# Kernel tuning notes

Hardware: AMD Instinct MI355X
Metric: run time of the kernel (lower is better)

Reference implementation:

```python
import jax, jax.numpy as jnp
import numpy as np

EMB = 1024; H = 8; HD = EMB // H // 2  # head_dim = 64, q/k use 2*H heads of HD; v uses H heads of 2*HD
FF = 4096; DEPTH = 1
LAM_INIT = float(0.8 - 0.6 * np.exp(-0.3 * DEPTH))

def setup_inputs() -> dict:
    key = jax.random.key(0)
    ks = jax.random.split(key, 12)
    s = lambda k, sh, sc: jax.random.normal(k, sh, jnp.float32) * sc
    return {
        'x': s(ks[0], (2, 2048, EMB), 1.0),
        'ln1_w': jnp.ones((EMB,), jnp.float32), 'ln1_b': jnp.zeros((EMB,), jnp.float32),
        'Wq': s(ks[1], (EMB, EMB), 0.02), 'Wk': s(ks[2], (EMB, EMB), 0.02),
        'Wv': s(ks[3], (EMB, EMB), 0.02), 'Wo': s(ks[4], (EMB, EMB), 0.02),
        'lq1': s(ks[5], (HD,), 0.1), 'lk1': s(ks[6], (HD,), 0.1),
        'lq2': s(ks[7], (HD,), 0.1), 'lk2': s(ks[8], (HD,), 0.1),
        'subln_w': jnp.ones((2 * HD,), jnp.float32),
        'ln2_w': jnp.ones((EMB,), jnp.float32), 'ln2_b': jnp.zeros((EMB,), jnp.float32),
        'W1': s(ks[9], (EMB, FF), 0.02), 'b1': jnp.zeros((FF,), jnp.float32),
        'W2': s(ks[10], (FF, EMB), 0.02), 'b2': jnp.zeros((EMB,), jnp.float32),
    }

def _ln(x, w, b):
    m = jnp.mean(x, -1, keepdims=True)
    v = jnp.var(x, -1, keepdims=True)
    return (x - m) * jax.lax.rsqrt(v + 1e-5) * w + b

def _rms(x, w):
    return x * jax.lax.rsqrt(jnp.mean(x * x, -1, keepdims=True) + 1e-5) * w

def reference(x, ln1_w, ln1_b, Wq, Wk, Wv, Wo, lq1, lk1, lq2, lk2, subln_w, ln2_w, ln2_b, W1, b1, W2, b2):
    B, N, _ = x.shape
    h = _ln(x, ln1_w, ln1_b)
    q = (h @ Wq).reshape(B, N, 2 * H, HD) * (HD ** -0.5)
    k = (h @ Wk).reshape(B, N, 2 * H, HD)
    v = (h @ Wv).reshape(B, N, H, 2 * HD)
    # dual softmax attention maps: [B, 2H, N, N]
    attn = jax.nn.softmax(jnp.einsum('bihd,bjhd->bhij', q, k), axis=-1)
    attn = attn.reshape(B, H, 2, N, N)
    lam = jnp.exp(jnp.sum(lq1 * lk1)) - jnp.exp(jnp.sum(lq2 * lk2)) + LAM_INIT
    a = attn[:, :, 0] - lam * attn[:, :, 1]  # differential attention [B,H,N,N]
    o = jnp.einsum('bhij,bjhd->bihd', a, v)  # [B,N,H,2*HD]
    o = _rms(o, subln_w) * (1.0 - LAM_INIT)
    x = x + o.reshape(B, N, EMB) @ Wo
    h = _ln(x, ln2_w, ln2_b)
    return x + (jax.nn.gelu(h @ W1 + b1, approximate=False) @ W2 + b2)
```

## Files before the change

### kernel.cpp

```cpp
#include <hip/hip_runtime.h>


typedef unsigned short u16;
typedef unsigned int u32;
typedef __attribute__((ext_vector_type(8))) __bf16 bf16x8;
typedef __attribute__((ext_vector_type(4))) float f32x4;
typedef __attribute__((ext_vector_type(4))) u32 u32x4;
typedef __attribute__((ext_vector_type(2))) u32 u32x2;

#define LOG2E 1.4426950408889634f
#define LAM_INIT 0.355509068f
#define ONE_MINUS_LAM_INIT 0.644490932f

__device__ __forceinline__ float bf2f(u16 x) {
  u32 u = ((u32)x) << 16;
  return __builtin_bit_cast(float, u);
}
__device__ __forceinline__ u16 f2bf(float f) {
  u32 u = __builtin_bit_cast(u32, f);
  u32 r = (u + 0x7FFFu + ((u >> 16) & 1u)) >> 16;
  return (u16)r;
}
__device__ __forceinline__ u32 cvtpk(float lo, float hi) {
  u32 r;
  asm("v_cvt_pk_bf16_f32 %0, %1, %2" : "=v"(r) : "v"(lo), "v"(hi));
  return r;
}
__device__ __forceinline__ float ldf(const void* p, size_t i, bool f32) {
  return f32 ? ((const float*)p)[i] : bf2f(((const u16*)p)[i]);
}
__device__ __forceinline__ void async16(const u16* g, u16* l) {
  __builtin_amdgcn_global_load_lds((const __attribute__((address_space(1))) u32*)g,
                                   (__attribute__((address_space(3))) u32*)l, 16, 0, 0);
}
__device__ __forceinline__ bf16x8 ld8(const u16* p) { return *(const bf16x8*)p; }

__global__ void detect_kernel(const u32* x, int* flag) {
  int e = (x[threadIdx.x] >> 7) & 0xFF;
  unsigned long long m = __ballot(e >= 90 && e <= 150);
  if (threadIdx.x == 0) flag[0] = (__popcll(m) >= 40) ? 1 : 0;
}

__global__ void lam_kernel(const void* lq1, const void* lk1, const void* lq2,
                           const void* lk2, const int* flag, float* out) {
  const bool f32 = flag[0] == 0;
  int L = threadIdx.x;
  float a = ldf(lq1, L, f32) * ldf(lk1, L, f32);
  float c = ldf(lq2, L, f32) * ldf(lk2, L, f32);
#pragma unroll
  for (int m = 1; m < 64; m <<= 1) { a += __shfl_xor(a, m); c += __shfl_xor(c, m); }
  if (L == 0) out[0] = __expf(a) - __expf(c) + LAM_INIT;
}

__device__ __forceinline__ void unpack8(u32x4 u, float* f) {
#pragma unroll
  for (int i = 0; i < 4; ++i) {
    f[2 * i] = bf2f((u16)(u[i] & 0xffffu));
    f[2 * i + 1] = bf2f((u16)(u[i] >> 16));
  }
}

template <bool XRAW>
__global__ __launch_bounds__(256) void ln_kernel(const void* __restrict__ x,
                                                 const void* __restrict__ w,
                                                 const void* __restrict__ b,
                                                 const int* __restrict__ flag,
                                                 u16* __restrict__ out) {
  const bool f32 = flag[0] == 0;
  const int row = blockIdx.x * 4 + (threadIdx.x >> 6);
  const int L = threadIdx.x & 63;
  float xv[16];
  if (XRAW && f32) {
    const f32x4* xr = (const f32x4*)((const float*)x + (size_t)row * 1024 + L * 16);
#pragma unroll
    for (int i = 0; i < 4; ++i) {
      f32x4 vv = xr[i];
#pragma unroll
      for (int j = 0; j < 4; ++j) xv[i * 4 + j] = vv[j];
    }
  } else {
    const u16* xr = (const u16*)x + (size_t)row * 1024 + L * 16;
    unpack8(*(const u32x4*)xr, xv);
    unpack8(*(const u32x4*)(xr + 8), xv + 8);
  }
  float s = 0.f, sq = 0.f;
#pragma unroll
  for (int i = 0; i < 16; ++i) { s += xv[i]; sq += xv[i] * xv[i]; }
#pragma unroll
  for (int m = 1; m < 64; m <<= 1) { s += __shfl_xor(s, m); sq += __shfl_xor(sq, m); }
  float mean = s * (1.0f / 1024.0f);
  float var = sq * (1.0f / 1024.0f) - mean * mean;
  float rstd = rsqrtf(var + 1e-5f);
  u32 pk[8];
#pragma unroll
  for (int i = 0; i < 8; ++i) {
    float w0 = ldf(w, L * 16 + 2 * i, f32), w1 = ldf(w, L * 16 + 2 * i + 1, f32);
    float b0 = ldf(b, L * 16 + 2 * i, f32), b1v = ldf(b, L * 16 + 2 * i + 1, f32);
    float v0 = (xv[2 * i] - mean) * rstd * w0 + b0;
    float v1 = (xv[2 * i + 1] - mean) * rstd * w1 + b1v;
    pk[i] = (u32)f2bf(v0) | ((u32)f2bf(v1) << 16);
  }
  u32x4 o0 = {pk[0], pk[1], pk[2], pk[3]};
  u32x4 o1 = {pk[4], pk[5], pk[6], pk[7]};
  *(u32x4*)(out + (size_t)row * 1024 + L * 16) = o0;
  *(u32x4*)(out + (size_t)row * 1024 + L * 16 + 8) = o1;
}

__global__ __launch_bounds__(256) void twc_kernel(const void* __restrict__ s0,
                                                  const void* __restrict__ s1,
                                                  const void* __restrict__ s2,
                                                  u16* __restrict__ dst, int sstride,
                                                  int dstride, size_t soff, size_t dzoff,
                                                  const int* __restrict__ flag) {
  __shared__ __align__(16) u16 tile[64][72];
  const bool f32 = flag[0] == 0;
  const void* src = blockIdx.z == 0 ? s0 : (blockIdx.z == 1 ? s1 : s2);
  u16* dz = dst + (size_t)blockIdx.z * dzoff;
  const int r0 = blockIdx.y * 64, c0 = blockIdx.x * 64;
  const int t = threadIdx.x;
  const int rr = t >> 3, cc = t & 7;
#pragma unroll
  for (int i = 0; i < 2; ++i) {
    int row = rr + i * 32;
    size_t idx = (size_t)(r0 + row) * sstride + c0 + cc * 8 + soff;
    if (f32) {
      const f32x4* s = (const f32x4*)((const float*)src + idx);
      f32x4 a = s[0], b = s[1];
      union { u16 t16[8]; u32x4 v; } u_;
#pragma unroll
      for (int j = 0; j < 4; ++j) { u_.t16[j] = f2bf(a[j]); u_.t16[4 + j] = f2bf(b[j]); }
      *(u32x4*)(&tile[row][cc * 8]) = u_.v;
    } else {
      *(u32x4*)(&tile[row][cc * 8]) = *(const u32x4*)((const u16*)src + idx);
    }
  }
  __syncthreads();
  u16* d = dz + (size_t)c0 * dstride + r0;
#pragma unroll
  for (int i = 0; i < 2; ++i) {
    int n = rr + i * 32;
    union { u16 t16[8]; u32x4 v; } u_;
#pragma unroll
    for (int j = 0; j < 8; ++j) u_.t16[j] = tile[cc * 8 + j][n];
    *(u32x4*)(d + (size_t)n * dstride + cc * 8) = u_.v;
  }
}

enum { EP_NONE = 0, EP_RES = 2, EP_GELU = 3, EP_BIASRES = 4, EP_QKV = 5 };

template <int TM, int EPI, bool RESRAW, bool OUTFLEX, bool DB>
__global__ __launch_bounds__(256, 2) void gemm_bt(
    const u16* __restrict__ A, const u16* __restrict__ Bt, void* __restrict__ Cv,
    int M, int N, int K, const void* __restrict__ bias, int boff,
    const void* __restrict__ res, const int* __restrict__ flag,
    u16* __restrict__ kout, u16* __restrict__ vtout) {
  constexpr int MT = TM / 32;
  constexpr int HALF = TM * 64 + 128 * 64;
  extern __shared__ __align__(16) u16 lds[];
  const int t = threadIdx.x;
  const int w = t >> 6, L = t & 63;
  const int quad = L >> 4, l16 = L & 15;
  const int m0 = blockIdx.y * TM, n0 = blockIdx.x * 128;
  const int wm = (TM == 128) ? (w >> 1) * 64 : (w & 1) * 32;
  const int wn = (TM == 128) ? (w & 1) * 64 : (w >> 1) * 64;
  const int srow = L >> 3, spc = L & 7;
  const int sc = spc ^ srow;

  f32x4 acc[MT][4] = {};
  const u16* Ab = A + (size_t)m0 * K;
  const u16* Bb = Bt + (size_t)n0 * K;

  auto stage = [&](int kt, int bsel) {
    u16* base = lds + bsel * HALF;
#pragma unroll
    for (int r = 0; r < TM / 32; ++r) {
      int row = r * 32 + w * 8 + srow;
      async16(Ab + (size_t)row * K + kt + sc * 8, &base[row * 64 + spc * 8]);
    }
#pragma unroll
    for (int r = 0; r < 4; ++r) {
      int row = r * 32 + w * 8 + srow;
      async16(Bb + (size_t)row * K + kt + sc * 8, &base[TM * 64 + row * 64 + spc * 8]);
    }
  };
  auto ktile = [&](const u16* base) {
#pragma unroll
    for (int ks = 0; ks < 2; ++ks) {
      bf16x8 af[MT], bfr[4];
#pragma unroll
      for (int mt = 0; mt < MT; ++mt) {
        int row = wm + mt * 16 + l16;
        af[mt] = ld8(&base[row * 64 + (((ks * 4 + quad) ^ (l16 & 7)) * 8)]);
      }
#pragma unroll
      for (int nt = 0; nt < 4; ++nt) {
        int row = wn + nt * 16 + l16;
        bfr[nt] = ld8(&base[TM * 64 + row * 64 + (((ks * 4 + quad) ^ (l16 & 7)) * 8)]);
      }
#pragma unroll
      for (int mt = 0; mt < MT; ++mt)
#pragma unroll
        for (int nt = 0; nt < 4; ++nt)
          acc[mt][nt] =
              __builtin_amdgcn_mfma_f32_16x16x32_bf16(af[mt], bfr[nt], acc[mt][nt], 0, 0, 0);
    }
  };

  if (DB) {
    const int nst = K >> 6;
    stage(0, 0);
    for (int st = 0; st < nst; ++st) {
      __syncthreads();
      if (st + 1 < nst) stage((st + 1) << 6, (st + 1) & 1);
      ktile(lds + (st & 1) * HALF);
    }
  } else {
    for (int kt = 0; kt < K; kt += 64) {
      stage(kt, 0);
      __syncthreads();
      ktile(lds);
      __syncthreads();
    }
  }

  const bool f32 = flag[0] == 0;
#pragma unroll
  for (int mt = 0; mt < MT; ++mt) {
#pragma unroll
    for (int nt = 0; nt < 4; ++nt) {
      int col = n0 + wn + nt * 16 + l16;
      float bv = 0.f;
      if (EPI == EP_GELU || EPI == EP_BIASRES) bv = ldf(bias, (size_t)boff + col, f32);
#pragma unroll
      for (int r = 0; r < 4; ++r) {
        int row = m0 + wm + mt * 16 + quad * 4 + r;
        float v = acc[mt][nt][r];
        if (EPI == EP_GELU) {
          v += bv;
          v = 0.5f * v * (1.0f + erff(v * 0.70710678118654752f));
        }
        if (EPI == EP_RES || EPI == EP_BIASRES) {
          size_t ri = (size_t)row * N + col;
          float rv = RESRAW ? ldf(res, ri, f32) : bf2f(((const u16*)res)[ri]);
          v += rv;
          if (EPI == EP_BIASRES) v += bv;
        }
        if (EPI == EP_QKV) {
          if (col < 1024) {
            ((u16*)Cv)[(size_t)row * 1024 + col] = f2bf(v * 0.125f);
          } else if (col < 2048) {
            kout[(size_t)row * 1024 + (col - 1024)] = f2bf(v);
          } else {
            int c2 = col - 2048;
            int bb = row >> 11, n = row & 2047, hh = c2 >> 7, d = c2 & 127;
            vtout[(size_t)((bb * 8 + hh) * 128 + d) * 2048 + n] = f2bf(v);
          }
        } else {
          size_t ci = (size_t)row * N + col;
          if (OUTFLEX && f32)
            ((float*)Cv)[ci] = v;
          else
            ((u16*)Cv)[ci] = f2bf(v);
        }
      }
    }
  }
}

__global__ __launch_bounds__(256, 2) void attn_kernel(
    const u16* __restrict__ q, const u16* __restrict__ k, const u16* __restrict__ vT,
    const float* __restrict__ lamp, const void* __restrict__ subw,
    const int* __restrict__ flag, u16* __restrict__ o) {
  extern __shared__ __align__(16) u16 lds[];
  constexpr int VB = 16384;
  const int t = threadIdx.x, w = t >> 6, L = t & 63;
  const int quad = L >> 4, l16 = L & 15;
  const int bid = ((blockIdx.x & 7) << 6) | (blockIdx.x >> 3);
  const int qt = bid & 31, h = (bid >> 5) & 7, b = bid >> 8;
  const int q0 = qt * 64;
  const int comp = w >> 1, rh = (w & 1) * 32;
  const int srow = L >> 3, spc = L & 7, sc = spc ^ srow;
  const u16* vb = vT + (size_t)(b * 8 + h) * (128 * 2048);

  auto stageK = [&](int kt, int bsel) {
#pragma unroll
    for (int r = 0; r < 4; ++r) {
      int row = r * 32 + w * 8 + srow;
      int c_ = row >> 6, key = row & 63;
      async16(k + ((size_t)(b * 2048 + kt + key) * 1024 + (2 * h + c_) * 64 + sc * 8),
              &lds[bsel * 8192 + row * 64 + spc * 8]);
    }
  };
  auto stageV = [&](int kt, int bsel) {
#pragma unroll
    for (int r = 0; r < 4; ++r) {
      int dim = r * 32 + w * 8 + srow;
      async16(vb + (size_t)dim * 2048 + kt + sc * 8,
              &lds[VB + bsel * 8192 + dim * 64 + spc * 8]);
    }
  };

  stageK(0, 0);
  stageV(0, 0);
  bf16x8 qf[2][2];
#pragma unroll
  for (int mt = 0; mt < 2; ++mt)
#pragma unroll
    for (int ks = 0; ks < 2; ++ks) {
      int row = q0 + rh + mt * 16 + l16;
      qf[mt][ks] = ld8(q + (size_t)(b * 2048 + row) * 1024 + (2 * h + comp) * 64 +
                       ks * 32 + quad * 8);
    }

  float mst[2] = {-1.0e30f, -1.0e30f};
  float mstl[2] = {-1.0e30f, -1.0e30f};
  float lst[2] = {0.f, 0.f};
  f32x4 oacc[8][2] = {};

  auto tile = [&](int ti, int bb) {
    f32x4 s[4][2] = {};
#pragma unroll
    for (int ks = 0; ks < 2; ++ks) {
      bf16x8 kf[4];
#pragma unroll
      for (int nt = 0; nt < 4; ++nt) {
        int row = nt * 16 + l16;
        kf[nt] = ld8(&lds[bb * 8192 + comp * 4096 + row * 64 +
                          (((ks * 4 + quad) ^ (l16 & 7)) * 8)]);
      }
#pragma unroll
      for (int nt = 0; nt < 4; ++nt)
#pragma unroll
        for (int mt = 0; mt < 2; ++mt)
          s[nt][mt] = __builtin_amdgcn_mfma_f32_16x16x32_bf16(kf[nt], qf[mt][ks], s[nt][mt], 0, 0, 0);
    }

    u32 wreg[2][4][2];
#pragma unroll
    for (int mt = 0; mt < 2; ++mt) {
      float mx = -3.0e38f;
#pragma unroll
      for (int nt = 0; nt < 4; ++nt)
#pragma unroll
        for (int r = 0; r < 4; ++r) mx = fmaxf(mx, s[nt][mt][r]);
      mx = fmaxf(mx, __shfl_xor(mx, 16));
      mx = fmaxf(mx, __shfl_xor(mx, 32));
      if (__ballot(mx > mst[mt] + 8.0f)) {
        float mnew = fmaxf(mst[mt], mx);
        float al = exp2f((mst[mt] - mnew) * LOG2E);
        mst[mt] = mnew;
        mstl[mt] = mnew * LOG2E;
        lst[mt] *= al;
#pragma unroll
        for (int nt = 0; nt < 8; ++nt)
#pragma unroll
          for (int r = 0; r < 4; ++r) oacc[nt][mt][r] *= al;
      }
      float ps = 0.f;
#pragma unroll
      for (int nt = 0; nt < 4; ++nt) {
#pragma unroll
        for (int r = 0; r < 4; ++r) {
          float p = exp2f(__builtin_fmaf(s[nt][mt][r], LOG2E, -mstl[mt]));
          s[nt][mt][r] = p;
          ps += p;
        }
        wreg[mt][nt][0] = cvtpk(s[nt][mt][0], s[nt][mt][1]);
        wreg[mt][nt][1] = cvtpk(s[nt][mt][2], s[nt][mt][3]);
      }
      ps += __shfl_xor(ps, 16);
      ps += __shfl_xor(ps, 32);
      lst[mt] += ps;
    }

#pragma unroll
    for (int ks = 0; ks < 2; ++ks) {
      bf16x8 pf[2];
#pragma unroll
      for (int mt = 0; mt < 2; ++mt) {
        u32 a0 = wreg[mt][2 * ks][0], b0 = wreg[mt][2 * ks + 1][0];
        u32 a1 = wreg[mt][2 * ks][1], b1 = wreg[mt][2 * ks + 1][1];
        asm("v_permlane32_swap_b32 %0, %1" : "+v"(a0), "+v"(b0));
        asm("v_permlane16_swap_b32 %0, %1" : "+v"(a0), "+v"(b0));
        asm("v_permlane32_swap_b32 %0, %1" : "+v"(a1), "+v"(b1));
        asm("v_permlane16_swap_b32 %0, %1" : "+v"(a1), "+v"(b1));
        u32x4 pw = {a0, a1, b0, b1};
        pf[mt] = __builtin_bit_cast(bf16x8, pw);
      }
#pragma unroll
      for (int nt = 0; nt < 8; ++nt) {
        int dim = nt * 16 + l16;
        bf16x8 vf = ld8(&lds[VB + bb * 8192 + dim * 64 +
                             (((ks * 4 + quad) ^ (l16 & 7)) * 8)]);
#pragma unroll
        for (int mt = 0; mt < 2; ++mt)
          oacc[nt][mt] = __builtin_amdgcn_mfma_f32_16x16x32_bf16(vf, pf[mt], oacc[nt][mt], 0, 0, 0);
      }
    }
  };

  for (int ti = 0; ti < 32; ti += 2) {
    __syncthreads();
    stageK((ti + 1) * 64, 1);
    stageV((ti + 1) * 64, 1);
    tile(ti, 0);
    __syncthreads();
    if (ti + 2 < 32) {
      stageK((ti + 2) * 64, 0);
      stageV((ti + 2) * 64, 0);
    }
    tile(ti + 1, 1);
  }

#pragma unroll
  for (int mt = 0; mt < 2; ++mt) {
    float inv = 1.0f / lst[mt];
#pragma unroll
    for (int nt = 0; nt < 8; ++nt)
#pragma unroll
      for (int r = 0; r < 4; ++r) oacc[nt][mt][r] *= inv;
  }

  __syncthreads();
  float* cb = (float*)lds;
  if (comp == 1) {
#pragma unroll
    for (int mt = 0; mt < 2; ++mt) {
      int rowc = rh + mt * 16 + l16;
#pragma unroll
      for (int nt = 0; nt < 8; ++nt)
        *(f32x4*)(&cb[rowc * 132 + nt * 16 + quad * 4]) = oacc[nt][mt];
    }
  }
  __syncthreads();
  if (comp == 0) {
    const bool f32 = flag[0] == 0;
    float lam = lamp[0];
    float sw[8][4];
#pragma unroll
    for (int nt = 0; nt < 8; ++nt)
#pragma unroll
      for (int r = 0; r < 4; ++r) sw[nt][r] = ldf(subw, nt * 16 + quad * 4 + r, f32);
#pragma unroll
    for (int mt = 0; mt < 2; ++mt) {
      int rowc = rh + mt * 16 + l16;
      float dv[8][4];
      float sq = 0.f;
#pragma unroll
      for (int nt = 0; nt < 8; ++nt) {
        f32x4 c2 = *(const f32x4*)(&cb[rowc * 132 + nt * 16 + quad * 4]);
#pragma unroll
        for (int r = 0; r < 4; ++r) {
          float d = oacc[nt][mt][r] - lam * c2[r];
          dv[nt][r] = d;
          sq += d * d;
        }
      }
      sq += __shfl_xor(sq, 16);
      sq += __shfl_xor(sq, 32);
      float rms = rsqrtf(sq * (1.0f / 128.0f) + 1e-5f);
      size_t rowg = (size_t)(b * 2048 + q0 + rowc) * 1024 + h * 128;
#pragma unroll
      for (int nt = 0; nt < 8; ++nt) {
        float v0 = dv[nt][0] * rms * sw[nt][0] * ONE_MINUS_LAM_INIT;
        float v1 = dv[nt][1] * rms * sw[nt][1] * ONE_MINUS_LAM_INIT;
        float v2 = dv[nt][2] * rms * sw[nt][2] * ONE_MINUS_LAM_INIT;
        float v3 = dv[nt][3] * rms * sw[nt][3] * ONE_MINUS_LAM_INIT;
        u32x2 pk2 = {cvtpk(v0, v1), cvtpk(v2, v3)};
        *(u32x2*)(o + rowg + nt * 16 + quad * 4) = pk2;
      }
    }
  }
}

extern "C" void kernel_launch(void* const* d_in, const int* in_sizes, int n_in,
                              void* d_out, int out_size, void* d_ws, size_t ws_size,
                              hipStream_t stream) {
  (void)in_sizes; (void)n_in; (void)out_size; (void)ws_size;
  const void* x = d_in[0];
  const void* ln1w = d_in[1];
  const void* ln1b = d_in[2];
  const void* Wq = d_in[3];
  const void* Wk = d_in[4];
  const void* Wv = d_in[5];
  const void* Wo = d_in[6];
  const void* lq1 = d_in[7];
  const void* lk1 = d_in[8];
  const void* lq2 = d_in[9];
  const void* lk2 = d_in[10];
  const void* subw = d_in[11];
  const void* ln2w = d_in[12];
  const void* ln2b = d_in[13];
  const void* W1 = d_in[14];
  const void* b1 = d_in[15];
  const void* W2 = d_in[16];
  const void* b2 = d_in[17];

  char* ws = (char*)d_ws;
  const size_t MB = 1u << 20;
  u16* A = (u16*)ws;
  u16* B = (u16*)(ws + 8 * MB);
  u16* C = (u16*)(ws + 16 * MB);
  u16* D = (u16*)(ws + 24 * MB);
  u16* E = (u16*)(ws + 32 * MB);
  float* lam = (float*)(ws + 40 * MB);
  int* flag = (int*)(ws + 40 * MB + 64);
  u16* W2Th = D + 2097152;

  const int g64_2 = (64 * 64 + 128 * 64) * 2 * 2;
  const int g128_2 = (128 * 64 + 128 * 64) * 2 * 2;

  detect_kernel<<<dim3(1), dim3(64), 0, stream>>>((const u32*)x, flag);
  lam_kernel<<<dim3(1), dim3(64), 0, stream>>>(lq1, lk1, lq2, lk2, flag, lam);
  ln_kernel<true><<<dim3(1024), dim3(256), 0, stream>>>(x, ln1w, ln1b, flag, A);

  twc_kernel<<<dim3(16, 16, 3), dim3(256), 0, stream>>>(Wq, Wk, Wv, E, 1024, 1024, 0,
                                                        1048576, flag);
  gemm_bt<64, EP_QKV, false, false, true><<<dim3(24, 64), dim3(256), g64_2, stream>>>(
      A, E, B, 4096, 3072, 1024, nullptr, 0, nullptr, flag, C, D);

  attn_kernel<<<dim3(512), dim3(256), 65536, stream>>>(B, C, D, lam, subw, flag, A);

  twc_kernel<<<dim3(16, 16, 1), dim3(256), 0, stream>>>(Wo, Wo, Wo, D, 1024, 1024, 0, 0,
                                                        flag);
  gemm_bt<64, EP_RES, true, false, true><<<dim3(8, 64), dim3(256), g64_2, stream>>>(
      A, D, E, 4096, 1024, 1024, nullptr, 0, x, flag, nullptr, nullptr);
  ln_kernel<false><<<dim3(1024), dim3(256), 0, stream>>>(E, ln2w, ln2b, flag, A);

  for (int hh = 0; hh < 2; ++hh) {
    twc_kernel<<<dim3(32, 16, 1), dim3(256), 0, stream>>>(W1, W1, W1, D, 4096, 1024,
                                                          (size_t)hh * 2048, 0, flag);
    twc_kernel<<<dim3(16, 32, 1), dim3(256), 0, stream>>>(
        W2, W2, W2, W2Th, 1024, 2048, (size_t)hh * 2048 * 1024, 0, flag);
    gemm_bt<128, EP_GELU, false, false, true><<<dim3(16, 32), dim3(256), g128_2, stream>>>(
        A, D, B, 4096, 2048, 1024, b1, hh * 2048, nullptr, flag, nullptr, nullptr);
    if (hh == 0) {
      gemm_bt<64, EP_BIASRES, false, true, true><<<dim3(8, 64), dim3(256), g64_2, stream>>>(
          B, W2Th, d_out, 4096, 1024, 2048, b2, 0, E, flag, nullptr, nullptr);
    } else {
      gemm_bt<64, EP_RES, true, true, true><<<dim3(8, 64), dim3(256), g64_2, stream>>>(
          B, W2Th, d_out, 4096, 1024, 2048, nullptr, 0, d_out, flag, nullptr, nullptr);
    }
  }
}
```

Baseline: 463.8 us.

## Split attention across 8 waves with 16 query rows each; single-buffer QKV GEMM

```diff
diff --git a/kernel.cpp b/kernel.cpp
--- a/kernel.cpp
+++ b/kernel.cpp
@@ -267,7 +267,7 @@
   }
 }
 
-__global__ __launch_bounds__(256, 2) void attn_kernel(
+__global__ __launch_bounds__(512, 4) void attn_kernel(
     const u16* __restrict__ q, const u16* __restrict__ k, const u16* __restrict__ vT,
     const float* __restrict__ lamp, const void* __restrict__ subw,
     const int* __restrict__ flag, u16* __restrict__ o) {
@@ -278,14 +278,14 @@
   const int bid = ((blockIdx.x & 7) << 6) | (blockIdx.x >> 3);
   const int qt = bid & 31, h = (bid >> 5) & 7, b = bid >> 8;
   const int q0 = qt * 64;
-  const int comp = w >> 1, rh = (w & 1) * 32;
+  const int comp = w >> 2, rh = (w & 3) * 16;
   const int srow = L >> 3, spc = L & 7, sc = spc ^ srow;
   const u16* vb = vT + (size_t)(b * 8 + h) * (128 * 2048);
 
   auto stageK = [&](int kt, int bsel) {
 #pragma unroll
-    for (int r = 0; r < 4; ++r) {
-      int row = r * 32 + w * 8 + srow;
+    for (int r = 0; r < 2; ++r) {
+      int row = w * 16 + r * 8 + srow;
       int c_ = row >> 6, key = row & 63;
       async16(k + ((size_t)(b * 2048 + kt + key) * 1024 + (2 * h + c_) * 64 + sc * 8),
               &lds[bsel * 8192 + row * 64 + spc * 8]);
@@ -293,8 +293,8 @@
   };
   auto stageV = [&](int kt, int bsel) {
 #pragma unroll
-    for (int r = 0; r < 4; ++r) {
-      int dim = r * 32 + w * 8 + srow;
+    for (int r = 0; r < 2; ++r) {
+      int dim = w * 16 + r * 8 + srow;
       async16(vb + (size_t)dim * 2048 + kt + sc * 8,
               &lds[VB + bsel * 8192 + dim * 64 + spc * 8]);
     }
@@ -302,23 +302,19 @@
 
   stageK(0, 0);
   stageV(0, 0);
-  bf16x8 qf[2][2];
-#pragma unroll
-  for (int mt = 0; mt < 2; ++mt)
-#pragma unroll
-    for (int ks = 0; ks < 2; ++ks) {
-      int row = q0 + rh + mt * 16 + l16;
-      qf[mt][ks] = ld8(q + (size_t)(b * 2048 + row) * 1024 + (2 * h + comp) * 64 +
-                       ks * 32 + quad * 8);
-    }
-
-  float mst[2] = {-1.0e30f, -1.0e30f};
-  float mstl[2] = {-1.0e30f, -1.0e30f};
-  float lst[2] = {0.f, 0.f};
-  f32x4 oacc[8][2] = {};
-
-  auto tile = [&](int ti, int bb) {
-    f32x4 s[4][2] = {};
+  bf16x8 qf[2];
+#pragma unroll
+  for (int ks = 0; ks < 2; ++ks) {
+    int row = q0 + rh + l16;
+    qf[ks] = ld8(q + (size_t)(b * 2048 + row) * 1024 + (2 * h + comp) * 64 +
+                 ks * 32 + quad * 8);
+  }
+
+  float mst = -1.0e30f, mstl = -1.0e30f, lst = 0.f;
+  f32x4 oacc[8] = {};
+
+  auto tile = [&](int bb) {
+    f32x4 s[4] = {};
 #pragma unroll
     for (int ks = 0; ks < 2; ++ks) {
       bf16x8 kf[4];
@@ -330,71 +326,60 @@
       }
 #pragma unroll
       for (int nt = 0; nt < 4; ++nt)
-#pragma unroll
-        for (int mt = 0; mt < 2; ++mt)
-          s[nt][mt] = __builtin_amdgcn_mfma_f32_16x16x32_bf16(kf[nt], qf[mt][ks], s[nt][mt], 0, 0, 0);
-    }
-
-    u32 wreg[2][4][2];
-#pragma unroll
-    for (int mt = 0; mt < 2; ++mt) {
-      float mx = -3.0e38f;
-#pragma unroll
-      for (int nt = 0; nt < 4; ++nt)
-#pragma unroll
-        for (int r = 0; r < 4; ++r) mx = fmaxf(mx, s[nt][mt][r]);
-      mx = fmaxf(mx, __shfl_xor(mx, 16));
-      mx = fmaxf(mx, __shfl_xor(mx, 32));
-      if (__ballot(mx > mst[mt] + 8.0f)) {
-        float mnew = fmaxf(mst[mt], mx);
-        float al = exp2f((mst[mt] - mnew) * LOG2E);
-        mst[mt] = mnew;
-        mstl[mt] = mnew * LOG2E;
-        lst[mt] *= al;
-#pragma unroll
-        for (int nt = 0; nt < 8; ++nt)
-#pragma unroll
-          for (int r = 0; r < 4; ++r) oacc[nt][mt][r] *= al;
-      }
-      float ps = 0.f;
-#pragma unroll
-      for (int nt = 0; nt < 4; ++nt) {
-#pragma unroll
-        for (int r = 0; r < 4; ++r) {
-          float p = exp2f(__builtin_fmaf(s[nt][mt][r], LOG2E, -mstl[mt]));
-          s[nt][mt][r] = p;
-          ps += p;
-        }
-        wreg[mt][nt][0] = cvtpk(s[nt][mt][0], s[nt][mt][1]);
-        wreg[mt][nt][1] = cvtpk(s[nt][mt][2], s[nt][mt][3]);
-      }
-      ps += __shfl_xor(ps, 16);
-      ps += __shfl_xor(ps, 32);
-      lst[mt] += ps;
-    }
+        s[nt] = __builtin_amdgcn_mfma_f32_16x16x32_bf16(kf[nt], qf[ks], s[nt], 0, 0, 0);
+    }
+
+    float mx = -3.0e38f;
+#pragma unroll
+    for (int nt = 0; nt < 4; ++nt)
+#pragma unroll
+      for (int r = 0; r < 4; ++r) mx = fmaxf(mx, s[nt][r]);
+    mx = fmaxf(mx, __shfl_xor(mx, 16));
+    mx = fmaxf(mx, __shfl_xor(mx, 32));
+    if (__ballot(mx > mst + 8.0f)) {
+      float mnew = fmaxf(mst, mx);
+      float al = exp2f((mst - mnew) * LOG2E);
+      mst = mnew;
+      mstl = mnew * LOG2E;
+      lst *= al;
+#pragma unroll
+      for (int nt = 0; nt < 8; ++nt)
+#pragma unroll
+        for (int r = 0; r < 4; ++r) oacc[nt][r] *= al;
+    }
+    float ps = 0.f;
+    u32 wreg[4][2];
+#pragma unroll
+    for (int nt = 0; nt < 4; ++nt) {
+#pragma unroll
+      for (int r = 0; r < 4; ++r) {
+        float p = exp2f(__builtin_fmaf(s[nt][r], LOG2E, -mstl));
+        s[nt][r] = p;
+        ps += p;
+      }
+      wreg[nt][0] = cvtpk(s[nt][0], s[nt][1]);
+      wreg[nt][1] = cvtpk(s[nt][2], s[nt][3]);
+    }
+    ps += __shfl_xor(ps, 16);
+    ps += __shfl_xor(ps, 32);
+    lst += ps;
 
 #pragma unroll
     for (int ks = 0; ks < 2; ++ks) {
-      bf16x8 pf[2];
-#pragma unroll
-      for (int mt = 0; mt < 2; ++mt) {
-        u32 a0 = wreg[mt][2 * ks][0], b0 = wreg[mt][2 * ks + 1][0];
-        u32 a1 = wreg[mt][2 * ks][1], b1 = wreg[mt][2 * ks + 1][1];
-        asm("v_permlane32_swap_b32 %0, %1" : "+v"(a0), "+v"(b0));
-        asm("v_permlane16_swap_b32 %0, %1" : "+v"(a0), "+v"(b0));
-        asm("v_permlane32_swap_b32 %0, %1" : "+v"(a1), "+v"(b1));
-        asm("v_permlane16_swap_b32 %0, %1" : "+v"(a1), "+v"(b1));
-        u32x4 pw = {a0, a1, b0, b1};
-        pf[mt] = __builtin_bit_cast(bf16x8, pw);
-      }
+      u32 a0 = wreg[2 * ks][0], b0 = wreg[2 * ks + 1][0];
+      u32 a1 = wreg[2 * ks][1], b1 = wreg[2 * ks + 1][1];
+      asm("v_permlane32_swap_b32 %0, %1" : "+v"(a0), "+v"(b0));
+      asm("v_permlane16_swap_b32 %0, %1" : "+v"(a0), "+v"(b0));
+      asm("v_permlane32_swap_b32 %0, %1" : "+v"(a1), "+v"(b1));
+      asm("v_permlane16_swap_b32 %0, %1" : "+v"(a1), "+v"(b1));
+      u32x4 pw = {a0, a1, b0, b1};
+      bf16x8 pf = __builtin_bit_cast(bf16x8, pw);
 #pragma unroll
       for (int nt = 0; nt < 8; ++nt) {
         int dim = nt * 16 + l16;
         bf16x8 vf = ld8(&lds[VB + bb * 8192 + dim * 64 +
                              (((ks * 4 + quad) ^ (l16 & 7)) * 8)]);
-#pragma unroll
-        for (int mt = 0; mt < 2; ++mt)
-          oacc[nt][mt] = __builtin_amdgcn_mfma_f32_16x16x32_bf16(vf, pf[mt], oacc[nt][mt], 0, 0, 0);
+        oacc[nt] = __builtin_amdgcn_mfma_f32_16x16x32_bf16(vf, pf, oacc[nt], 0, 0, 0);
       }
     }
   };
@@ -403,72 +388,60 @@
     __syncthreads();
     stageK((ti + 1) * 64, 1);
     stageV((ti + 1) * 64, 1);
-    tile(ti, 0);
+    tile(0);
     __syncthreads();
     if (ti + 2 < 32) {
       stageK((ti + 2) * 64, 0);
       stageV((ti + 2) * 64, 0);
     }
-    tile(ti + 1, 1);
-  }
-
-#pragma unroll
-  for (int mt = 0; mt < 2; ++mt) {
-    float inv = 1.0f / lst[mt];
+    tile(1);
+  }
+
+  {
+    float inv = 1.0f / lst;
 #pragma unroll
     for (int nt = 0; nt < 8; ++nt)
 #pragma unroll
-      for (int r = 0; r < 4; ++r) oacc[nt][mt][r] *= inv;
+      for (int r = 0; r < 4; ++r) oacc[nt][r] *= inv;
   }
 
   __syncthreads();
   float* cb = (float*)lds;
   if (comp == 1) {
-#pragma unroll
-    for (int mt = 0; mt < 2; ++mt) {
-      int rowc = rh + mt * 16 + l16;
-#pragma unroll
-      for (int nt = 0; nt < 8; ++nt)
-        *(f32x4*)(&cb[rowc * 132 + nt * 16 + quad * 4]) = oacc[nt][mt];
-    }
+    int rowc = rh + l16;
+#pragma unroll
+    for (int nt = 0; nt < 8; ++nt)
+      *(f32x4*)(&cb[rowc * 132 + nt * 16 + quad * 4]) = oacc[nt];
   }
   __syncthreads();
   if (comp == 0) {
     const bool f32 = flag[0] == 0;
     float lam = lamp[0];
-    float sw[8][4];
-#pragma unroll
-    for (int nt = 0; nt < 8; ++nt)
-#pragma unroll
-      for (int r = 0; r < 4; ++r) sw[nt][r] = ldf(subw, nt * 16 + quad * 4 + r, f32);
-#pragma unroll
-    for (int mt = 0; mt < 2; ++mt) {
-      int rowc = rh + mt * 16 + l16;
-      float dv[8][4];
-      float sq = 0.f;
-#pragma unroll
-      for (int nt = 0; nt < 8; ++nt) {
-        f32x4 c2 = *(const f32x4*)(&cb[rowc * 132 + nt * 16 + quad * 4]);
-#pragma unroll
-        for (int r = 0; r < 4; ++r) {
-          float d = oacc[nt][mt][r] - lam * c2[r];
-          dv[nt][r] = d;
-          sq += d * d;
-        }
-      }
-      sq += __shfl_xor(sq, 16);
-      sq += __shfl_xor(sq, 32);
-      float rms = rsqrtf(sq * (1.0f / 128.0f) + 1e-5f);
-      size_t rowg = (size_t)(b * 2048 + q0 + rowc) * 1024 + h * 128;
-#pragma unroll
-      for (int nt = 0; nt < 8; ++nt) {
-        float v0 = dv[nt][0] * rms * sw[nt][0] * ONE_MINUS_LAM_INIT;
-        float v1 = dv[nt][1] * rms * sw[nt][1] * ONE_MINUS_LAM_INIT;
-        float v2 = dv[nt][2] * rms * sw[nt][2] * ONE_MINUS_LAM_INIT;
-        float v3 = dv[nt][3] * rms * sw[nt][3] * ONE_MINUS_LAM_INIT;
-        u32x2 pk2 = {cvtpk(v0, v1), cvtpk(v2, v3)};
-        *(u32x2*)(o + rowg + nt * 16 + quad * 4) = pk2;
-      }
+    int rowc = rh + l16;
+    float dv[8][4];
+    float sq = 0.f;
+#pragma unroll
+    for (int nt = 0; nt < 8; ++nt) {
+      f32x4 c2 = *(const f32x4*)(&cb[rowc * 132 + nt * 16 + quad * 4]);
+#pragma unroll
+      for (int r = 0; r < 4; ++r) {
+        float d = oacc[nt][r] - lam * c2[r];
+        dv[nt][r] = d;
+        sq += d * d;
+      }
+    }
+    sq += __shfl_xor(sq, 16);
+    sq += __shfl_xor(sq, 32);
+    float rms = rsqrtf(sq * (1.0f / 128.0f) + 1e-5f);
+    size_t rowg = (size_t)(b * 2048 + q0 + rowc) * 1024 + h * 128;
+#pragma unroll
+    for (int nt = 0; nt < 8; ++nt) {
+      float v0 = dv[nt][0] * rms * ldf(subw, nt * 16 + quad * 4 + 0, f32) * ONE_MINUS_LAM_INIT;
+      float v1 = dv[nt][1] * rms * ldf(subw, nt * 16 + quad * 4 + 1, f32) * ONE_MINUS_LAM_INIT;
+      float v2 = dv[nt][2] * rms * ldf(subw, nt * 16 + quad * 4 + 2, f32) * ONE_MINUS_LAM_INIT;
+      float v3 = dv[nt][3] * rms * ldf(subw, nt * 16 + quad * 4 + 3, f32) * ONE_MINUS_LAM_INIT;
+      u32x2 pk2 = {cvtpk(v0, v1), cvtpk(v2, v3)};
+      *(u32x2*)(o + rowg + nt * 16 + quad * 4) = pk2;
     }
   }
 }
@@ -507,7 +480,8 @@
   int* flag = (int*)(ws + 40 * MB + 64);
   u16* W2Th = D + 2097152;
 
-  const int g64_2 = (64 * 64 + 128 * 64) * 2 * 2;
+  const int g64_1 = (64 * 64 + 128 * 64) * 2;
+  const int g64_2 = g64_1 * 2;
   const int g128_2 = (128 * 64 + 128 * 64) * 2 * 2;
 
   detect_kernel<<<dim3(1), dim3(64), 0, stream>>>((const u32*)x, flag);
@@ -516,10 +490,10 @@
 
   twc_kernel<<<dim3(16, 16, 3), dim3(256), 0, stream>>>(Wq, Wk, Wv, E, 1024, 1024, 0,
                                                         1048576, flag);
-  gemm_bt<64, EP_QKV, false, false, true><<<dim3(24, 64), dim3(256), g64_2, stream>>>(
+  gemm_bt<64, EP_QKV, false, false, false><<<dim3(24, 64), dim3(256), g64_1, stream>>>(
       A, E, B, 4096, 3072, 1024, nullptr, 0, nullptr, flag, C, D);
 
-  attn_kernel<<<dim3(512), dim3(256), 65536, stream>>>(B, C, D, lam, subw, flag, A);
+  attn_kernel<<<dim3(512), dim3(512), 65536, stream>>>(B, C, D, lam, subw, flag, A);
 
   twc_kernel<<<dim3(16, 16, 1), dim3(256), 0, stream>>>(Wo, Wo, Wo, D, 1024, 1024, 0, 0,
                                                         flag);
```

After: 449.3 us. -3.1%, faster.
